# Kernel optimization log

Hardware: AMD Instinct MI355X
Metric: run time of the kernel (lower is better)

## Reference

```python
import jax, jax.numpy as jnp
import numpy as np

S, B, D, E, F = 2048, 2, 1024, 8, 4096


def setup_inputs() -> dict:
    key = jax.random.key(0)
    ks = jax.random.split(key, 6)
    x = jax.random.normal(ks[0], (S, B, D), dtype=jnp.float32)
    w_switch = jax.random.normal(ks[1], (D, E), dtype=jnp.float32) / np.sqrt(D)
    b_switch = jnp.zeros((E,), dtype=jnp.float32)
    w1 = jax.random.normal(ks[2], (E, D, F), dtype=jnp.float32) / np.sqrt(D)
    b1 = jnp.zeros((E, F), dtype=jnp.float32)
    w2 = jax.random.normal(ks[3], (E, F, D), dtype=jnp.float32) / np.sqrt(F)
    b2 = jnp.zeros((E, D), dtype=jnp.float32)
    return {"x": x, "w_switch": w_switch, "b_switch": b_switch,
            "w1": w1, "b1": b1, "w2": w2, "b2": b2}


def reference(x, w_switch, b_switch, w1, b1, w2, b2):
    # x: [S, B, D] -> tokens [N, D]
    s, b, d = x.shape
    n_experts = w1.shape[0]
    xf = x.reshape(-1, d)                                    # [N, D]
    route_prob = jax.nn.softmax(xf @ w_switch + b_switch, axis=-1)  # [N, E]
    route_prob_max = jnp.max(route_prob, axis=-1)            # [N]
    routes = jnp.argmax(route_prob, axis=-1)                 # [N] int
    # is_scale_prob=True: scale token by its routing probability before FFN
    xs = xf * route_prob_max[:, None]                        # [N, D]
    # Per-expert FFN evaluated densely (drop_tokens=False => every token kept),
    # then each token selects its routed expert's output.
    h = jax.nn.relu(jnp.einsum('nd,edf->enf', xs, w1) + b1[:, None, :])  # [E, N, F]
    y = jnp.einsum('enf,efd->end', h, w2) + b2[:, None, :]               # [E, N, D]
    n = xf.shape[0]
    out = y[routes, jnp.arange(n)]                           # [N, D]
    counts = jnp.zeros((n_experts,), dtype=jnp.float32).at[routes].add(1.0)
    n_dropped = jnp.zeros((), dtype=jnp.int32)               # drop_tokens=False
    return out.reshape(s, b, d), counts, route_prob.sum(0), n_dropped
```

## Files before the change

### kernel.cpp

```cpp
#include <hip/hip_runtime.h>
#include <hip/hip_bf16.h>

#define NTOK 4096
#define DDIM 1024
#define NEXP 8
#define FDIM 4096
#define MAXTILES 40

typedef __attribute__((ext_vector_type(4))) float f32x4;
typedef __attribute__((ext_vector_type(8))) short bf16x8;
typedef __attribute__((ext_vector_type(8))) unsigned short u16x8;

#define GLDS(g, l) __builtin_amdgcn_global_load_lds( \
    (const __attribute__((address_space(1))) unsigned int*)(g), \
    (__attribute__((address_space(3))) unsigned int*)(l), 16, 0, 0)

__global__ __launch_bounds__(256) void route_kernel(
    const float* __restrict__ x,
    const float* __restrict__ w_switch,
    const float* __restrict__ b_switch,
    __hip_bfloat16* __restrict__ xs,
    int* __restrict__ amax_arr,
    float* __restrict__ partial)
{
    const int tid = threadIdx.x;
    const int wave = tid >> 6, lane = tid & 63;
    __shared__ float pr[4][16];

    float wacc[16];
#pragma unroll
    for (int j = 0; j < 16; j++) wacc[j] = 0.0f;

    for (int i = 0; i < 4; i++) {
        const int n = blockIdx.x * 16 + wave * 4 + i;
        const float4* xr = (const float4*)(x + (size_t)n * DDIM);
        float4 xv[4];
#pragma unroll
        for (int j = 0; j < 4; j++) xv[j] = xr[lane + j * 64];

        float acc[NEXP];
#pragma unroll
        for (int e = 0; e < NEXP; e++) acc[e] = 0.0f;
#pragma unroll
        for (int j = 0; j < 4; j++) {
            const int dbase = (lane + j * 64) * 4;
#pragma unroll
            for (int c = 0; c < 4; c++) {
                const float4* wr = (const float4*)(w_switch + (size_t)(dbase + c) * NEXP);
                float4 w0 = wr[0], w1 = wr[1];
                float xvc = ((const float*)&xv[j])[c];
                acc[0] += xvc * w0.x; acc[1] += xvc * w0.y;
                acc[2] += xvc * w0.z; acc[3] += xvc * w0.w;
                acc[4] += xvc * w1.x; acc[5] += xvc * w1.y;
                acc[6] += xvc * w1.z; acc[7] += xvc * w1.w;
            }
        }
#pragma unroll
        for (int e = 0; e < NEXP; e++) {
            float v = acc[e];
#pragma unroll
            for (int off = 32; off > 0; off >>= 1) v += __shfl_xor(v, off, 64);
            acc[e] = v;
        }
        float mx = -1e30f;
#pragma unroll
        for (int e = 0; e < NEXP; e++) {
            acc[e] += b_switch[e];
            mx = fmaxf(mx, acc[e]);
        }
        float sum = 0.0f;
#pragma unroll
        for (int e = 0; e < NEXP; e++) { acc[e] = __expf(acc[e] - mx); sum += acc[e]; }
        float inv = 1.0f / sum;
        float pmax = -1.0f; int amax = 0;
#pragma unroll
        for (int e = 0; e < NEXP; e++) {
            float p = acc[e] * inv;
            acc[e] = p;
            if (p > pmax) { pmax = p; amax = e; }
        }
#pragma unroll
        for (int e = 0; e < NEXP; e++) {
            wacc[e] += acc[e];
            wacc[8 + e] += (amax == e) ? 1.0f : 0.0f;
        }
        if (lane == 0) amax_arr[n] = amax;
#pragma unroll
        for (int j = 0; j < 4; j++) {
            ushort4 pk;
            __hip_bfloat16* pp = (__hip_bfloat16*)&pk;
            pp[0] = __float2bfloat16(xv[j].x * pmax);
            pp[1] = __float2bfloat16(xv[j].y * pmax);
            pp[2] = __float2bfloat16(xv[j].z * pmax);
            pp[3] = __float2bfloat16(xv[j].w * pmax);
            *(ushort4*)(xs + (size_t)n * DDIM + (lane + j * 64) * 4) = pk;
        }
    }
    if (lane == 0) {
#pragma unroll
        for (int j = 0; j < 16; j++) pr[wave][j] = wacc[j];
    }
    __syncthreads();
    if (tid < 16)
        partial[blockIdx.x * 16 + tid] = pr[0][tid] + pr[1][tid] + pr[2][tid] + pr[3][tid];
}

__global__ __launch_bounds__(1024) void bucket_kernel(
    const int* __restrict__ amax_arr, int* __restrict__ bucket, int* __restrict__ ecnt)
{
    const int e = blockIdx.x;
    __shared__ int ctr;
    if (threadIdx.x == 0) ctr = 0;
    __syncthreads();
    const int lane = threadIdx.x & 63;
    for (int c = 0; c < NTOK; c += 1024) {
        int t = c + threadIdx.x;
        bool my = (amax_arr[t] == e);
        unsigned long long mask = __ballot(my);
        int cnt = __popcll(mask);
        int base = 0;
        if (lane == 0 && cnt) base = atomicAdd(&ctr, cnt);
        base = __shfl(base, 0, 64);
        if (my) {
            int rank = __popcll(mask & ((1ull << lane) - 1ull));
            bucket[e * NTOK + base + rank] = t;
        }
    }
    __syncthreads();
    if (threadIdx.x == 0) ecnt[e] = ctr;
}

__global__ __launch_bounds__(256) void finalize_table_kernel(
    const float* __restrict__ partial, const int* __restrict__ ecnt,
    float* __restrict__ out_tail, int* __restrict__ table)
{
    __shared__ float red[16][16];
    const int j = threadIdx.x & 15, g = threadIdx.x >> 4;
    float s = 0.0f;
    for (int k = 0; k < 16; k++) s += partial[(size_t)(g + k * 16) * 16 + j];
    red[g][j] = s;
    __syncthreads();
    if (threadIdx.x < 16) {
        float t = 0.0f;
        for (int k = 0; k < 16; k++) t += red[k][threadIdx.x];
        int dst = (threadIdx.x < 8) ? (8 + threadIdx.x) : (threadIdx.x - 8);
        out_tail[dst] = t;
    }
    if (threadIdx.x == 16) out_tail[16] = 0.0f;
    if (threadIdx.x == 0) {
        int idx = 0;
        for (int e = 0; e < NEXP; e++) {
            int cnt = ecnt[e];
            for (int m0 = 0; m0 < cnt; m0 += 128) table[idx++] = (e << 16) | m0;
        }
        for (; idx < MAXTILES; idx++) table[idx] = -1;
    }
}

template <int R, int C>
__global__ __launch_bounds__(256) void transpose_kernel(
    const float* __restrict__ in, __hip_bfloat16* __restrict__ outp)
{
    const int e = blockIdx.z;
    const int r0 = blockIdx.y * 64, c0 = blockIdx.x * 64;
    __shared__ __hip_bfloat16 t[64 * 65];
    const int tid = threadIdx.x;
    const int ri = tid >> 4, c4 = (tid & 15) * 4;
    const float* src = in + ((size_t)e * R + r0) * C + c0;
#pragma unroll
    for (int rr = 0; rr < 4; rr++) {
        int r = ri + rr * 16;
        float4 v = *(const float4*)(src + (size_t)r * C + c4);
        t[r * 65 + c4 + 0] = __float2bfloat16(v.x);
        t[r * 65 + c4 + 1] = __float2bfloat16(v.y);
        t[r * 65 + c4 + 2] = __float2bfloat16(v.z);
        t[r * 65 + c4 + 3] = __float2bfloat16(v.w);
    }
    __syncthreads();
    const int co = tid >> 2, m = tid & 3;
    u16x8 v0, v1;
#pragma unroll
    for (int idx = 0; idx < 8; idx++)
        ((unsigned short*)&v0)[idx] = *(const unsigned short*)&t[(m * 16 + idx) * 65 + co];
#pragma unroll
    for (int idx = 0; idx < 8; idx++)
        ((unsigned short*)&v1)[idx] = *(const unsigned short*)&t[(m * 16 + idx + 8) * 65 + co];
    __hip_bfloat16* dst = outp + ((size_t)e * C + c0 + co) * R + r0 + m * 16;
    *(u16x8*)(dst) = v0;
    *(u16x8*)(dst + 8) = v1;
}

template <int MODE, int K, int NN, int KS, int NX>
__device__ __forceinline__ void gemm_body(
    const __hip_bfloat16* __restrict__ A,
    const __hip_bfloat16* __restrict__ Bt,
    const float* __restrict__ bias,
    const int* __restrict__ bucket,
    const int* __restrict__ ecnt,
    const int* __restrict__ table,
    void* __restrict__ Out)
{
    const int bid = blockIdx.x;
    const int xcd = bid & 7;
    const int q = bid >> 3;
    const int x = q % NX;
    const int yk = (q / NX) % (MAXTILES / 8);
    const int z = q / (NX * (MAXTILES / 8));
    const int y = xcd + 8 * yk;

    const int entry = table[y];
    if (entry < 0) return;
    const int e = entry >> 16;
    const int m0 = entry & 0xffff;
    const int cnt = ecnt[e];
    const int n0 = x * 128;
    const int kbase = (K / KS) * z;

    __shared__ __align__(16) __hip_bfloat16 Asm[128 * 64];
    __shared__ __align__(16) __hip_bfloat16 Bsm[128 * 64];
    __shared__ int toks[128];

    const int tid = threadIdx.x;
    if (tid < 128) {
        int r = m0 + tid;
        toks[tid] = bucket[e * NTOK + (r < cnt ? r : cnt - 1)];
    }
    __syncthreads();

    const int wave = tid >> 6, lane = tid & 63;
    const int srow = lane >> 3;
    const int swzcol = ((lane & 7) ^ srow) * 16;

    const char* pA[4];
#pragma unroll
    for (int i = 0; i < 4; i++)
        pA[i] = (const char*)(A + (size_t)toks[wave * 32 + i * 8 + srow] * K + kbase) + swzcol;
    const char* pB = (const char*)(Bt + ((size_t)e * NN + n0 + wave * 32 + srow) * K + kbase) + swzcol;

    const int wm = wave & 1, wn = wave >> 1;
    const int r16 = lane & 15, kq16 = lane >> 4;
    const int r7x = (r16 & 7) * 16;

    f32x4 acc[4][4];
#pragma unroll
    for (int t = 0; t < 4; t++)
#pragma unroll
        for (int u = 0; u < 4; u++) acc[t][u] = (f32x4){0.f, 0.f, 0.f, 0.f};

    for (int k0 = 0; k0 < K / KS; k0 += 64) {
#pragma unroll
        for (int i = 0; i < 4; i++) {
            GLDS(pA[i], (char*)Asm + (wave * 32 + i * 8) * 128 + lane * 16);
            GLDS(pB + (size_t)i * 8 * K * 2, (char*)Bsm + (wave * 32 + i * 8) * 128 + lane * 16);
            pA[i] += 128;
        }
        pB += 128;
        __syncthreads();

#pragma unroll
        for (int ksub = 0; ksub < 2; ksub++) {
            const int slot = ((kq16 + ksub * 4) * 16) ^ r7x;
            bf16x8 a[4], b[4];
#pragma unroll
            for (int t = 0; t < 4; t++)
                a[t] = *(const bf16x8*)((const char*)Asm +
                        (wm * 64 + t * 16 + r16) * 128 + slot);
#pragma unroll
            for (int u = 0; u < 4; u++)
                b[u] = *(const bf16x8*)((const char*)Bsm +
                        (wn * 64 + u * 16 + r16) * 128 + slot);
#pragma unroll
            for (int t = 0; t < 4; t++)
#pragma unroll
                for (int u = 0; u < 4; u++)
                    acc[t][u] = __builtin_amdgcn_mfma_f32_16x16x32_bf16(a[t], b[u], acc[t][u], 0, 0, 0);
        }
        __syncthreads();
    }

    const int quad = lane >> 4, l15 = lane & 15;
    float bv[4];
#pragma unroll
    for (int u = 0; u < 4; u++) {
        if (MODE == 0)
            bv[u] = bias[(size_t)e * NN + n0 + wn * 64 + u * 16 + l15];
        else
            bv[u] = (z == 0) ? bias[(size_t)e * NN + n0 + wn * 64 + u * 16 + l15] : 0.0f;
    }
#pragma unroll
    for (int t = 0; t < 4; t++) {
#pragma unroll
        for (int rr = 0; rr < 4; rr++) {
            int row = wm * 64 + t * 16 + quad * 4 + rr;
            if (m0 + row < cnt) {
                int tok = toks[row];
#pragma unroll
                for (int u = 0; u < 4; u++) {
                    int col = n0 + wn * 64 + u * 16 + l15;
                    float v = acc[t][u][rr] + bv[u];
                    if (MODE == 0) {
                        v = fmaxf(v, 0.0f);
                        ((__hip_bfloat16*)Out)[(size_t)tok * NN + col] = __float2bfloat16(v);
                    } else {
                        unsafeAtomicAdd(&((float*)Out)[(size_t)tok * NN + col], v);
                    }
                }
            }
        }
    }
}

__global__ __launch_bounds__(256, 4) void gemm_ffn1(
    const __hip_bfloat16* __restrict__ A, const __hip_bfloat16* __restrict__ Bt,
    const float* __restrict__ bias, const int* __restrict__ bucket,
    const int* __restrict__ ecnt, const int* __restrict__ table, void* __restrict__ Out)
{
    gemm_body<0, DDIM, FDIM, 1, FDIM / 128>(A, Bt, bias, bucket, ecnt, table, Out);
}

__global__ __launch_bounds__(256, 4) void gemm_ffn2(
    const __hip_bfloat16* __restrict__ A, const __hip_bfloat16* __restrict__ Bt,
    const float* __restrict__ bias, const int* __restrict__ bucket,
    const int* __restrict__ ecnt, const int* __restrict__ table, void* __restrict__ Out)
{
    gemm_body<1, FDIM, DDIM, 4, DDIM / 128>(A, Bt, bias, bucket, ecnt, table, Out);
}

extern "C" void kernel_launch(void* const* d_in, const int* in_sizes, int n_in,
                              void* d_out, int out_size, void* d_ws, size_t ws_size,
                              hipStream_t stream) {
    const float* x        = (const float*)d_in[0];
    const float* w_switch = (const float*)d_in[1];
    const float* b_switch = (const float*)d_in[2];
    const float* w1       = (const float*)d_in[3];
    const float* b1       = (const float*)d_in[4];
    const float* w2       = (const float*)d_in[5];
    const float* b2       = (const float*)d_in[6];

    float* out = (float*)d_out;
    float* out_tail = out + (size_t)NTOK * DDIM;

    char* ws = (char*)d_ws;
    __hip_bfloat16* xs = (__hip_bfloat16*)(ws);
    __hip_bfloat16* h  = (__hip_bfloat16*)(ws + 8388608ull);
    __hip_bfloat16* wt = (__hip_bfloat16*)(ws + 41943040ull);
    int* bucket        = (int*)(ws + 109051904ull);
    int* amax_arr      = (int*)(ws + 109182976ull);
    float* partial     = (float*)(ws + 109199360ull);
    int* ecnt          = (int*)(ws + 109215744ull);
    int* table         = (int*)(ws + 109215776ull);

    hipMemsetAsync(out, 0, (size_t)NTOK * DDIM * sizeof(float), stream);

    hipLaunchKernelGGL(route_kernel, dim3(256), dim3(256), 0, stream,
                       x, w_switch, b_switch, xs, amax_arr, partial);
    hipLaunchKernelGGL(bucket_kernel, dim3(NEXP), dim3(1024), 0, stream,
                       amax_arr, bucket, ecnt);
    hipLaunchKernelGGL(finalize_table_kernel, dim3(1), dim3(256), 0, stream,
                       partial, ecnt, out_tail, table);

    hipLaunchKernelGGL((transpose_kernel<DDIM, FDIM>), dim3(FDIM / 64, DDIM / 64, NEXP),
                       dim3(256), 0, stream, w1, wt);
    hipLaunchKernelGGL(gemm_ffn1, dim3((FDIM / 128) * MAXTILES), dim3(256), 0, stream,
                       xs, wt, b1, bucket, ecnt, table, (void*)h);

    hipLaunchKernelGGL((transpose_kernel<FDIM, DDIM>), dim3(DDIM / 64, FDIM / 64, NEXP),
                       dim3(256), 0, stream, w2, wt);
    hipLaunchKernelGGL(gemm_ffn2, dim3((DDIM / 128) * MAXTILES * 4), dim3(256), 0, stream,
                       h, wt, b2, bucket, ecnt, table, (void*)out);
}
```

Baseline: 481.9 us.

## Merge bucket and finalize kernels; retile weight transpose to 128x128 with swizzled LDS

The per-expert bucket kernel and the finalize/table kernel are combined into one 1024-thread block that loops over all experts, which saves a launch and a dependency step. The weight transpose kernel now uses 128x128 tiles. It writes to LDS with an XOR swizzle instead of padding, reads 16-byte vectors, and repacks with byte-permute instructions so each global write is a full 16-byte store. The aim is cheaper LDS traffic and wider memory transactions in the transpose, which runs over 64M weights per call. In exchange, each block uses 32KB of LDS and holds more registers.

```diff
diff --git a/kernel.cpp b/kernel.cpp
--- a/kernel.cpp
+++ b/kernel.cpp
@@ -9,7 +9,6 @@
 
 typedef __attribute__((ext_vector_type(4))) float f32x4;
 typedef __attribute__((ext_vector_type(8))) short bf16x8;
-typedef __attribute__((ext_vector_type(8))) unsigned short u16x8;
 
 #define GLDS(g, l) __builtin_amdgcn_global_load_lds( \
     (const __attribute__((address_space(1))) unsigned int*)(g), \
@@ -105,53 +104,53 @@
         partial[blockIdx.x * 16 + tid] = pr[0][tid] + pr[1][tid] + pr[2][tid] + pr[3][tid];
 }
 
-__global__ __launch_bounds__(1024) void bucket_kernel(
-    const int* __restrict__ amax_arr, int* __restrict__ bucket, int* __restrict__ ecnt)
-{
-    const int e = blockIdx.x;
-    __shared__ int ctr;
-    if (threadIdx.x == 0) ctr = 0;
+__global__ __launch_bounds__(1024) void bucket_finalize_kernel(
+    const int* __restrict__ amax_arr, const float* __restrict__ partial,
+    int* __restrict__ bucket, int* __restrict__ ecnt,
+    float* __restrict__ out_tail, int* __restrict__ table)
+{
+    __shared__ int ctr[NEXP];
+    __shared__ float red[16][16];
+    if (threadIdx.x < NEXP) ctr[threadIdx.x] = 0;
     __syncthreads();
     const int lane = threadIdx.x & 63;
     for (int c = 0; c < NTOK; c += 1024) {
         int t = c + threadIdx.x;
-        bool my = (amax_arr[t] == e);
-        unsigned long long mask = __ballot(my);
-        int cnt = __popcll(mask);
-        int base = 0;
-        if (lane == 0 && cnt) base = atomicAdd(&ctr, cnt);
-        base = __shfl(base, 0, 64);
-        if (my) {
-            int rank = __popcll(mask & ((1ull << lane) - 1ull));
-            bucket[e * NTOK + base + rank] = t;
-        }
-    }
-    __syncthreads();
-    if (threadIdx.x == 0) ecnt[e] = ctr;
-}
-
-__global__ __launch_bounds__(256) void finalize_table_kernel(
-    const float* __restrict__ partial, const int* __restrict__ ecnt,
-    float* __restrict__ out_tail, int* __restrict__ table)
-{
-    __shared__ float red[16][16];
-    const int j = threadIdx.x & 15, g = threadIdx.x >> 4;
-    float s = 0.0f;
-    for (int k = 0; k < 16; k++) s += partial[(size_t)(g + k * 16) * 16 + j];
-    red[g][j] = s;
-    __syncthreads();
+        int a = amax_arr[t];
+#pragma unroll
+        for (int e = 0; e < NEXP; e++) {
+            bool my = (a == e);
+            unsigned long long mask = __ballot(my);
+            int cnt = __popcll(mask);
+            int base = 0;
+            if (lane == 0 && cnt) base = atomicAdd(&ctr[e], cnt);
+            base = __shfl(base, 0, 64);
+            if (my) {
+                int rank = __popcll(mask & ((1ull << lane) - 1ull));
+                bucket[e * NTOK + base + rank] = t;
+            }
+        }
+    }
+    if (threadIdx.x < 256) {
+        const int j = threadIdx.x & 15, g = threadIdx.x >> 4;
+        float s = 0.0f;
+        for (int k = 0; k < 16; k++) s += partial[(size_t)(g + k * 16) * 16 + j];
+        red[g][j] = s;
+    }
+    __syncthreads();
+    if (threadIdx.x < NEXP) ecnt[threadIdx.x] = ctr[threadIdx.x];
     if (threadIdx.x < 16) {
-        float t = 0.0f;
-        for (int k = 0; k < 16; k++) t += red[k][threadIdx.x];
+        float t2 = 0.0f;
+        for (int k = 0; k < 16; k++) t2 += red[k][threadIdx.x];
         int dst = (threadIdx.x < 8) ? (8 + threadIdx.x) : (threadIdx.x - 8);
-        out_tail[dst] = t;
+        out_tail[dst] = t2;
     }
     if (threadIdx.x == 16) out_tail[16] = 0.0f;
     if (threadIdx.x == 0) {
         int idx = 0;
         for (int e = 0; e < NEXP; e++) {
-            int cnt = ecnt[e];
-            for (int m0 = 0; m0 < cnt; m0 += 128) table[idx++] = (e << 16) | m0;
+            int cnt2 = ctr[e];
+            for (int m0 = 0; m0 < cnt2; m0 += 128) table[idx++] = (e << 16) | m0;
         }
         for (; idx < MAXTILES; idx++) table[idx] = -1;
     }
@@ -162,32 +161,43 @@
     const float* __restrict__ in, __hip_bfloat16* __restrict__ outp)
 {
     const int e = blockIdx.z;
-    const int r0 = blockIdx.y * 64, c0 = blockIdx.x * 64;
-    __shared__ __hip_bfloat16 t[64 * 65];
+    const int r0 = blockIdx.y * 128, c0 = blockIdx.x * 128;
+    __shared__ __align__(16) __hip_bfloat16 t[128 * 128];
     const int tid = threadIdx.x;
-    const int ri = tid >> 4, c4 = (tid & 15) * 4;
+
     const float* src = in + ((size_t)e * R + r0) * C + c0;
 #pragma unroll
-    for (int rr = 0; rr < 4; rr++) {
-        int r = ri + rr * 16;
-        float4 v = *(const float4*)(src + (size_t)r * C + c4);
-        t[r * 65 + c4 + 0] = __float2bfloat16(v.x);
-        t[r * 65 + c4 + 1] = __float2bfloat16(v.y);
-        t[r * 65 + c4 + 2] = __float2bfloat16(v.z);
-        t[r * 65 + c4 + 3] = __float2bfloat16(v.w);
-    }
-    __syncthreads();
-    const int co = tid >> 2, m = tid & 3;
-    u16x8 v0, v1;
-#pragma unroll
-    for (int idx = 0; idx < 8; idx++)
-        ((unsigned short*)&v0)[idx] = *(const unsigned short*)&t[(m * 16 + idx) * 65 + co];
-#pragma unroll
-    for (int idx = 0; idx < 8; idx++)
-        ((unsigned short*)&v1)[idx] = *(const unsigned short*)&t[(m * 16 + idx + 8) * 65 + co];
-    __hip_bfloat16* dst = outp + ((size_t)e * C + c0 + co) * R + r0 + m * 16;
-    *(u16x8*)(dst) = v0;
-    *(u16x8*)(dst + 8) = v1;
+    for (int k = 0; k < 16; k++) {
+        const int id = k * 256 + tid;
+        const int row = id >> 5, colq = id & 31;
+        float4 v = *(const float4*)(src + (size_t)row * C + colq * 4);
+        ushort4 pk;
+        __hip_bfloat16* pp = (__hip_bfloat16*)&pk;
+        pp[0] = __float2bfloat16(v.x); pp[1] = __float2bfloat16(v.y);
+        pp[2] = __float2bfloat16(v.z); pp[3] = __float2bfloat16(v.w);
+        const int b = (row * 256 + colq * 8) ^ (((row >> 3) & 1) << 6);
+        *(ushort4*)((char*)t + b) = pk;
+    }
+    __syncthreads();
+
+    const int rb = tid & 15, cb = tid >> 4;
+    unsigned v[8][4];
+#pragma unroll
+    for (int i = 0; i < 8; i++) {
+        const int row = rb * 8 + i;
+        const int b = (row * 256 + cb * 16) ^ ((rb & 1) << 6);
+        *(uint4*)v[i] = *(const uint4*)((const char*)t + b);
+    }
+    __hip_bfloat16* dst = outp + ((size_t)e * C + c0 + cb * 8) * R + r0 + rb * 8;
+#pragma unroll
+    for (int j = 0; j < 8; j++) {
+        const unsigned sel = (j & 1) ? 0x07060302u : 0x05040100u;
+        unsigned o[4];
+#pragma unroll
+        for (int w = 0; w < 4; w++)
+            o[w] = __builtin_amdgcn_perm(v[2 * w + 1][j >> 1], v[2 * w][j >> 1], sel);
+        *(uint4*)(dst + (size_t)j * R) = *(uint4*)o;
+    }
 }
 
 template <int MODE, int K, int NN, int KS, int NX>
@@ -354,17 +364,15 @@
 
     hipLaunchKernelGGL(route_kernel, dim3(256), dim3(256), 0, stream,
                        x, w_switch, b_switch, xs, amax_arr, partial);
-    hipLaunchKernelGGL(bucket_kernel, dim3(NEXP), dim3(1024), 0, stream,
-                       amax_arr, bucket, ecnt);
-    hipLaunchKernelGGL(finalize_table_kernel, dim3(1), dim3(256), 0, stream,
-                       partial, ecnt, out_tail, table);
-
-    hipLaunchKernelGGL((transpose_kernel<DDIM, FDIM>), dim3(FDIM / 64, DDIM / 64, NEXP),
+    hipLaunchKernelGGL(bucket_finalize_kernel, dim3(1), dim3(1024), 0, stream,
+                       amax_arr, partial, bucket, ecnt, out_tail, table);
+
+    hipLaunchKernelGGL((transpose_kernel<DDIM, FDIM>), dim3(FDIM / 128, DDIM / 128, NEXP),
                        dim3(256), 0, stream, w1, wt);
     hipLaunchKernelGGL(gemm_ffn1, dim3((FDIM / 128) * MAXTILES), dim3(256), 0, stream,
                        xs, wt, b1, bucket, ecnt, table, (void*)h);
 
-    hipLaunchKernelGGL((transpose_kernel<FDIM, DDIM>), dim3(DDIM / 64, FDIM / 64, NEXP),
+    hipLaunchKernelGGL((transpose_kernel<FDIM, DDIM>), dim3(DDIM / 128, FDIM / 128, NEXP),
                        dim3(256), 0, stream, w2, wt);
     hipLaunchKernelGGL(gemm_ffn2, dim3((DDIM / 128) * MAXTILES * 4), dim3(256), 0, stream,
                        h, wt, b2, bucket, ecnt, table, (void*)out);
```

After: 480.8 us. No clear change (-0.2%).
